# Kernel tuning notes

Measured on AMD Instinct MI355X. Metric: run time of the kernel, lower is better.

The kernel has to match this reference:

```python
import jax, jax.numpy as jnp
import numpy as np
from jax import lax

S, B, D_IN, H, T = 512, 256, 202, 100, 19  # seq, batch, input, hidden, tags


def setup_inputs() -> dict:
    key = jax.random.key(0)
    ks = jax.random.split(key, 16)
    sc = 0.1
    inp = {
        "x": jax.random.normal(ks[0], (S, B, D_IN), dtype=jnp.float32),
        "y": jax.random.randint(ks[1], (S, B), 0, T, dtype=jnp.int64),
        # forward-direction RNN params
        "W_ih_f": jax.random.normal(ks[2], (H, D_IN), dtype=jnp.float32) * sc,
        "W_hh_f": jax.random.normal(ks[3], (H, H), dtype=jnp.float32) * sc,
        "b_ih_f": jax.random.normal(ks[4], (H,), dtype=jnp.float32) * sc,
        "b_hh_f": jax.random.normal(ks[5], (H,), dtype=jnp.float32) * sc,
        # backward-direction RNN params
        "W_ih_b": jax.random.normal(ks[6], (H, D_IN), dtype=jnp.float32) * sc,
        "W_hh_b": jax.random.normal(ks[7], (H, H), dtype=jnp.float32) * sc,
        "b_ih_b": jax.random.normal(ks[8], (H,), dtype=jnp.float32) * sc,
        "b_hh_b": jax.random.normal(ks[9], (H,), dtype=jnp.float32) * sc,
        # tag projection
        "W_tag": jax.random.normal(ks[10], (T, 2 * H), dtype=jnp.float32) * sc,
        "b_tag": jax.random.normal(ks[11], (T,), dtype=jnp.float32) * sc,
        # CRF params
        "start_trans": jax.random.normal(ks[12], (T,), dtype=jnp.float32) * sc,
        "end_trans": jax.random.normal(ks[13], (T,), dtype=jnp.float32) * sc,
        "trans": jax.random.normal(ks[14], (T, T), dtype=jnp.float32) * sc,
    }
    return inp


def _rnn_dir(x, Wih, Whh, bih, bhh):
    # x: (S, B, D_IN) -> hs: (S, B, H), vanilla tanh RNN
    xp = jnp.einsum('sbd,hd->sbh', x, Wih) + bih + bhh
    h0 = jnp.zeros((x.shape[1], Wih.shape[0]), dtype=x.dtype)

    def step(h, xt):
        h = jnp.tanh(xt + h @ Whh.T)
        return h, h

    _, hs = lax.scan(step, h0, xp)
    return hs


def _crf_llh(emissions, tags, start_trans, end_trans, trans):
    # emissions: (N, L, T) batch_first; tags: (N, L). Returns sum log-likelihood.
    N, L, _ = emissions.shape
    # numerator: score of gold path
    em_score = jnp.take_along_axis(emissions, tags[..., None], axis=2)[..., 0].sum(axis=1)  # (N,)
    tr_score = trans[tags[:, :-1], tags[:, 1:]].sum(axis=1)  # (N,)
    numerator = start_trans[tags[:, 0]] + em_score + tr_score + end_trans[tags[:, -1]]
    # denominator: forward algorithm (log partition)
    alpha0 = start_trans + emissions[:, 0]  # (N, T)
    em_rest = jnp.swapaxes(emissions, 0, 1)[1:]  # (L-1, N, T)

    def step(alpha, em_t):
        # alpha: (N, T); broadcast over next-tag axis
        alpha = jax.nn.logsumexp(alpha[:, :, None] + trans[None] + em_t[:, None, :], axis=1)
        return alpha, None

    alpha, _ = lax.scan(step, alpha0, em_rest)
    denominator = jax.nn.logsumexp(alpha + end_trans, axis=1)  # (N,)
    return jnp.sum(numerator - denominator)


def reference(x, y, W_ih_f, W_hh_f, b_ih_f, b_hh_f, W_ih_b, W_hh_b, b_ih_b, b_hh_b,
              W_tag, b_tag, start_trans, end_trans, trans):
    # bidirectional RNN (seq-first, as nn.RNN default)
    h_fwd = _rnn_dir(x, W_ih_f, W_hh_f, b_ih_f, b_hh_f)
    h_bwd = _rnn_dir(x[::-1], W_ih_b, W_hh_b, b_ih_b, b_hh_b)[::-1]
    h = jnp.concatenate([h_fwd, h_bwd], axis=-1)  # (S, B, 200)
    logits = jnp.einsum('sbh,th->sbt', h, W_tag) + b_tag  # (S, B, 19)
    probs = jax.nn.softmax(logits, axis=2)
    # CRF was constructed with batch_first=True, so the (S,B,19) tensor is
    # treated as batch=S, seq=B (faithful to the original module's behavior).
    return _crf_llh(probs, y, start_trans, end_trans, trans)
```

## Files before the change

### kernel.cpp

```cpp
#include <hip/hip_runtime.h>
#include <math.h>

#define SS 512
#define BB 256
#define DIN 202
#define HH 100
#define TT 19

typedef short short8 __attribute__((ext_vector_type(8)));
typedef float f32x4 __attribute__((ext_vector_type(4)));

#define MFMA16(A, B, C) __builtin_amdgcn_mfma_f32_16x16x32_bf16(A, B, C, 0, 0, 0)

__device__ __forceinline__ float rl(float v, int i) {
    return __int_as_float(__builtin_amdgcn_readlane(__float_as_int(v), i));
}
__device__ __forceinline__ float rfl(float v) {
    return __int_as_float(__builtin_amdgcn_readfirstlane(__float_as_int(v)));
}
__device__ __forceinline__ unsigned short f2bf(float f) {
  unsigned u = __float_as_uint(f);
  u += 0x7fff + ((u >> 16) & 1);
  return (unsigned short)(u >> 16);
}
__device__ __forceinline__ float bf2f(unsigned v) {
  return __int_as_float((int)(v << 16));
}
__device__ __forceinline__ float fast_tanh(float z) {
  float e = __expf(2.f * z);
  return (e - 1.f) * __fdividef(1.f, e + 1.f);
}
__device__ __forceinline__ void gl_lds16(const void* g, void* l) {
  __builtin_amdgcn_global_load_lds(
      (const __attribute__((address_space(1))) unsigned int*)g,
      (__attribute__((address_space(3))) unsigned int*)l, 16, 0, 0);
}
__device__ __forceinline__ unsigned cvt_pk_bf16(float lo, float hi) {
  unsigned r;
  asm("v_cvt_pk_bf16_f32 %0, %1, %2" : "=v"(r) : "v"(lo), "v"(hi));
  return r;
}
__device__ __forceinline__ uint2 pack_tanh_pk(f32x4 a) {
  float h0 = fast_tanh(a[0]), h1 = fast_tanh(a[1]);
  float h2 = fast_tanh(a[2]), h3 = fast_tanh(a[3]);
  uint2 v;
  v.x = cvt_pk_bf16(h0, h1);
  v.y = cvt_pk_bf16(h2, h3);
  return v;
}
__device__ __forceinline__ uint2 pack_raw_pk(f32x4 a) {
  uint2 v;
  v.x = cvt_pk_bf16(a[0], a[1]);
  v.y = cvt_pk_bf16(a[2], a[3]);
  return v;
}
__device__ __forceinline__ f32x4 seed_from(const void* base, int off) {
  uint2 s = *(const uint2*)((const char*)base + off);
  return (f32x4){bf2f(s.x & 0xffffu), bf2f(s.x >> 16),
                 bf2f(s.y & 0xffffu), bf2f(s.y >> 16)};
}

__global__ __launch_bounds__(256) void k_cvtW(
    const float* __restrict__ Wf, const float* __restrict__ Wb,
    unsigned short* __restrict__ Wfrag) {
  int w = blockIdx.x * 256 + threadIdx.x;
  if (w >= 7 * 13 * 64) return;
  int kc = w / (13 * 64);
  int r = w % (13 * 64);
  int ft = r >> 6, l = r & 63;
  int nn = ft * 16 + (l & 15);
  int kb = kc * 32 + (l >> 4) * 8;
  union { unsigned short s[8]; int4 v; } pk;
  #pragma unroll
  for (int e = 0; e < 8; ++e) {
    int k = kb + e;
    float vv = 0.f;
    if (k < DIN) {
      if (nn < 100) vv = Wf[(size_t)nn * DIN + k];
      else if (nn < 200) vv = Wb[(size_t)(nn - 100) * DIN + k];
    }
    pk.s[e] = f2bf(vv);
  }
  *(int4*)&Wfrag[(size_t)w * 8] = pk.v;
}

__global__ __launch_bounds__(256) void k_inproj(
    const float* __restrict__ x, const unsigned short* __restrict__ Wfrag,
    const float* __restrict__ bihf, const float* __restrict__ bhhf,
    const float* __restrict__ bihb, const float* __restrict__ bhhb,
    unsigned short* __restrict__ xpT0, unsigned short* __restrict__ xpT1) {
  __shared__ __align__(16) char smem_raw[28672];
  __shared__ float lbias[208];
  short* lA = (short*)smem_raw;
  short* lB = (short*)(smem_raw + 8192);
  const int t = threadIdx.x;
  const int m0 = blockIdx.x * 128;
  const int s_idx = m0 >> 8;
  const int bhalf = (m0 >> 7) & 1;
  const int wv = t >> 6, lane = t & 63;
  const int li = lane & 15;

  if (t < 208) {
    float bv = 0.f;
    if (t < 100) bv = bihf[t] + bhhf[t];
    else if (t < 200) bv = bihb[t - 100] + bhhb[t - 100];
    lbias[t] = bv;
  }

  f32x4 acc[2][13];
  #pragma unroll
  for (int mf = 0; mf < 2; ++mf)
    #pragma unroll
    for (int nf = 0; nf < 13; ++nf)
      acc[mf][nf] = (f32x4){0.f, 0.f, 0.f, 0.f};

  for (int kc = 0; kc < 7; ++kc) {
    const int k0 = kc * 32;
    __syncthreads();
    #pragma unroll
    for (int j = 0; j < 8; ++j) {
      int g = t + 256 * j;
      int row = g >> 4, cp = g & 15;
      int col = k0 + cp * 2;
      unsigned pk2 = 0;
      if (col + 1 < DIN) {
        float2 v = *(const float2*)(x + (size_t)(m0 + row) * DIN + col);
        pk2 = cvt_pk_bf16(v.x, v.y);
      }
      int ft = row >> 4, i = row & 15;
      int kq = cp >> 2, e = (cp & 3) * 2;
      *(unsigned*)&lA[ft * 512 + (kq * 16 + i) * 8 + e] = pk2;
    }
    #pragma unroll
    for (int i = 0; i < 4; ++i) {
      int j = i * 4 + wv;
      if (j < 13)
        gl_lds16(Wfrag + ((size_t)(kc * 13 + j)) * 512, &lB[j * 512]);
    }
    __syncthreads();
    short8 a0 = *(const short8*)&lA[(2 * wv + 0) * 512 + lane * 8];
    short8 a1 = *(const short8*)&lA[(2 * wv + 1) * 512 + lane * 8];
    #pragma unroll
    for (int nf = 0; nf < 13; ++nf) {
      short8 b = *(const short8*)&lB[nf * 512 + lane * 8];
      acc[0][nf] = MFMA16(a0, b, acc[0][nf]);
      acc[1][nf] = MFMA16(a1, b, acc[1][nf]);
    }
  }
  __syncthreads();
  unsigned short* ep = (unsigned short*)smem_raw;
  float biasv[13];
  #pragma unroll
  for (int nf = 0; nf < 13; ++nf) biasv[nf] = lbias[nf * 16 + li];
  const int r0 = (lane >> 4) * 4;
  #pragma unroll
  for (int d = 0; d < 2; ++d) {
    if (d == 1) __syncthreads();
    #pragma unroll
    for (int mf = 0; mf < 2; ++mf) {
      int lrb = (2 * wv + mf) * 16 + r0;
      #pragma unroll
      for (int nf = 0; nf < 13; ++nf) {
        int col = nf * 16 + li;
        int c = col - 100 * d;
        if (c >= 0 && c < 100) {
          #pragma unroll
          for (int r = 0; r < 4; ++r)
            ep[(lrb + r) * 112 + c] = f2bf(acc[mf][nf][r] + biasv[nf]);
        }
      }
    }
    __syncthreads();
    unsigned short* dst0 = d ? xpT1 : xpT0;
    #pragma unroll
    for (int it = 0; it < 7; ++it) {
      int u = t + 256 * it;
      if (u < 1664) {
        int bgrpL = u / 208;
        int rem = u - bgrpL * 208;
        int u8 = rem >> 4, nn = rem & 15;
        int lr = bgrpL * 16 + nn;
        int4 v = *(const int4*)&ep[lr * 112 + u8 * 8];
        size_t off = ((((size_t)s_idx * 16 + bhalf * 8 + bgrpL) * 13 + u8) * 16 + nn) * 8;
        *(int4*)(dst0 + off) = v;
      }
    }
  }
}

__global__ __launch_bounds__(576) void k_rnn(
    const unsigned short* __restrict__ xpT0, const unsigned short* __restrict__ xpT1,
    const float* __restrict__ Whf, const float* __restrict__ Whb,
    const float* __restrict__ Wtag, float* __restrict__ plogF, float* __restrict__ plogB) {
  const int bid = blockIdx.x;
  const int dir = bid & 1;
  const int bgrp = (bid >> 1) & 15;
  const int b0 = bgrp * 16;
  const int seg = bid >> 5;
  const int start = (seg == 0) ? 0 : (64 * seg - 32);
  const int nch = (64 * seg + 64 - start) >> 3;
  const int outbase = 64 * seg;

  const float* Whh = dir ? Whb : Whf;
  const unsigned short* xpX = dir ? xpT1 : xpT0;
  float* plog = dir ? plogB : plogF;

  __shared__ short ringc[9][3][512];
  __shared__ short ring3[9][128];
  __shared__ unsigned short xpl[13312];
  __shared__ unsigned short larc[8 * 16 * 20];
  __shared__ short dummy16[8];

  const int t = threadIdx.x;
  const int wv = t >> 6, lane = t & 63;
  const int n = lane & 15, q = lane >> 4;

  for (int i = t; i < 3 * 512; i += 576) ringc[0][i >> 9][i & 511] = 0;
  for (int i = t; i < 9 * 128; i += 576) ring3[i >> 7][i & 127] = 0;
  if (t < 8) dummy16[t] = 0;

  short8 af[4];
  #pragma unroll
  for (int q2 = 0; q2 < 4; ++q2) af[q2] = (short8){0,0,0,0,0,0,0,0};
  {
    const float* base = nullptr;
    if (wv < 7) {
      int m = 16 * wv + n;
      if (m < HH) base = Whh + (size_t)m * HH;
    } else if (wv == 7) {
      if (n < TT) base = Wtag + (size_t)n * (2 * HH) + dir * HH;
    } else {
      int tA = 16 + n;
      if (tA < TT) base = Wtag + (size_t)tA * (2 * HH) + dir * HH;
    }
    #pragma unroll
    for (int q2 = 0; q2 < 4; ++q2) {
      union { unsigned short s[8]; short8 v; } pa;
      #pragma unroll
      for (int e = 0; e < 8; ++e) {
        int k = 32 * q2 + 8 * q + e;
        pa.s[e] = (base && k < HH) ? f2bf(base[k]) : 0;
      }
      af[q2] = pa.v;
    }
  }

  int slj[3], remj[3];
  #pragma unroll
  for (int i = 0; i < 3; ++i) {
    int j = i * 9 + wv;
    int jj = (j < 26) ? j : 0;
    int unit = jj * 64 + lane;
    slj[i] = unit / 208;
    remj[i] = unit - slj[i] * 208;
  }

  const int offW = ((2 * wv + (q >> 1)) * 16 + n) * 16 + (q & 1) * 8;

  for (int cc = 0; cc < nch; ++cc) {
    if (cc > 0) {
      if (t < 128) {
        int sl = t >> 4, nn2 = t & 15;
        int hs = start + (cc - 1) * 8 - 1 + sl;
        if (hs >= outbase) {
          int pos = dir ? (511 - hs) : hs;
          float* dst = plog + ((size_t)pos * 256 + b0 + nn2) * 20;
          const unsigned short* src = &larc[(sl * 16 + nn2) * 20];
          #pragma unroll
          for (int j5 = 0; j5 < 5; ++j5) {
            uint2 rv = *(const uint2*)&src[j5 * 4];
            float4 o;
            o.x = bf2f(rv.x & 0xffffu); o.y = bf2f(rv.x >> 16);
            o.z = bf2f(rv.y & 0xffffu); o.w = bf2f(rv.y >> 16);
            *(float4*)&dst[j5 * 4] = o;
          }
        }
      }
      if (t < 192) {
        *(int4*)&ringc[0][t >> 6][(t & 63) * 8] = *(const int4*)&ringc[8][t >> 6][(t & 63) * 8];
      } else if (t < 208) {
        int i2 = t - 192;
        *(int4*)&ring3[0][i2 * 8] = *(const int4*)&ring3[8][i2 * 8];
      }
    }
    #pragma unroll
    for (int i = 0; i < 3; ++i) {
      int j = i * 9 + wv;
      if (j < 26) {
        int s = start + cc * 8 + slj[i];
        int sq = dir ? (511 - s) : s;
        gl_lds16(xpX + (((size_t)sq * 16 + bgrp) * 208 + remj[i]) * 8, &xpl[j * 512]);
      }
    }
    __syncthreads();

    #pragma unroll
    for (int sl = 0; sl < 8; ++sl) {
      short8 hc0 = *(const short8*)&ringc[sl][0][lane * 8];
      short8 hc1 = *(const short8*)&ringc[sl][1][lane * 8];
      short8 hc2 = *(const short8*)&ringc[sl][2][lane * 8];
      short8 hc3 = *(const short8*)((q == 0) ? &ring3[sl][n * 8] : &dummy16[0]);
      f32x4 z4 = {0.f, 0.f, 0.f, 0.f};
      if (wv < 7) {
        int oW = sl * 3328 + offW;
        if (oW > 26616) oW = 26616;
        f32x4 seed = seed_from(xpl, oW);
        f32x4 a0 = MFMA16(af[0], hc0, seed);
        f32x4 a1 = MFMA16(af[1], hc1, z4);
        a0 = MFMA16(af[2], hc2, a0);
        a1 = MFMA16(af[3], hc3, a1);
        f32x4 a = a0 + a1;
        uint2 val = pack_tanh_pk(a);
        if (wv < 6) {
          *(uint2*)&ringc[sl + 1][wv >> 1][((2 * (wv & 1) + (q >> 1)) * 16 + n) * 8 + 4 * (q & 1)] = val;
        } else if (q == 0) {
          *(uint2*)&ring3[sl + 1][n * 8] = val;
        }
      } else {
        f32x4 a0 = MFMA16(af[0], hc0, z4);
        f32x4 a1 = MFMA16(af[1], hc1, z4);
        a0 = MFMA16(af[2], hc2, a0);
        a1 = MFMA16(af[3], hc3, a1);
        f32x4 a = a0 + a1;
        uint2 v = pack_raw_pk(a);
        if (wv == 7) {
          *(uint2*)&larc[(sl * 16 + n) * 20 + 4 * q] = v;
        } else if (q == 0) {
          *(uint2*)&larc[(sl * 16 + n) * 20 + 16] = v;
        }
      }
      __syncthreads();
    }
  }
  {
    if (t < 128) {
      int sl = t >> 4, nn2 = t & 15;
      int hs = start + (nch - 1) * 8 - 1 + sl;
      if (hs >= outbase) {
        int pos = dir ? (511 - hs) : hs;
        float* dst = plog + ((size_t)pos * 256 + b0 + nn2) * 20;
        const unsigned short* src = &larc[(sl * 16 + nn2) * 20];
        #pragma unroll
        for (int j5 = 0; j5 < 5; ++j5) {
          uint2 rv = *(const uint2*)&src[j5 * 4];
          float4 o;
          o.x = bf2f(rv.x & 0xffffu); o.y = bf2f(rv.x >> 16);
          o.z = bf2f(rv.y & 0xffffu); o.w = bf2f(rv.y >> 16);
          *(float4*)&dst[j5 * 4] = o;
        }
      }
    }
  }
  if (wv >= 7) {
    short8 hc0 = *(const short8*)&ringc[8][0][lane * 8];
    short8 hc1 = *(const short8*)&ringc[8][1][lane * 8];
    short8 hc2 = *(const short8*)&ringc[8][2][lane * 8];
    short8 hc3 = *(const short8*)((q == 0) ? &ring3[8][n * 8] : &dummy16[0]);
    f32x4 z4 = {0.f, 0.f, 0.f, 0.f};
    f32x4 a0 = MFMA16(af[0], hc0, z4);
    f32x4 a1 = MFMA16(af[1], hc1, z4);
    a0 = MFMA16(af[2], hc2, a0);
    a1 = MFMA16(af[3], hc3, a1);
    f32x4 a = a0 + a1;
    int hs = start + nch * 8 - 1;
    int pos = dir ? (511 - hs) : hs;
    float* dst = plog + ((size_t)pos * 256 + b0 + n) * 20;
    if (wv == 7) {
      #pragma unroll
      for (int r = 0; r < 4; ++r) dst[4 * q + r] = a[r];
    } else if (q == 0) {
      #pragma unroll
      for (int r = 0; r < 4; ++r) dst[16 + r] = a[r];
    }
  }
}

__global__ __launch_bounds__(256) void k_crf(
    const float* __restrict__ plogF, const float* __restrict__ plogB,
    const float* __restrict__ btag, const int* __restrict__ y,
    const float* __restrict__ start, const float* __restrict__ endt,
    const float* __restrict__ trans, float* __restrict__ out) {
  __shared__ float ltr[TT * TT];
  __shared__ float ltb[20];
  __shared__ float lem[4][64 * 21];
  const int t = threadIdx.x;
  const int wave = t >> 6, lane = t & 63;
  const int n = blockIdx.x * 4 + wave;
  for (int i = t; i < TT * TT; i += 256) ltr[i] = trans[i];
  if (t < 20) ltb[t] = (t < TT) ? btag[t] : 0.f;
  __syncthreads();
  const int* yn = y + n * BB;
  float Ereg[TT];
  #pragma unroll
  for (int i = 0; i < TT; ++i) Ereg[i] = (lane < TT) ? __expf(ltr[i * TT + lane]) : 0.f;
  float num = 0.f;
  float alpha = -1e30f;
  for (int c = 0; c < 4; ++c) {
    const size_t gbase = ((size_t)n * BB + c * 64) * 20;
    for (int u = lane; u < 1280; u += 64) {
      int row = u / 20, col = u - row * 20;
      lem[wave][row * 21 + col] = plogF[gbase + u] + plogB[gbase + u] + ltb[col];
    }
    {
      float vv[TT];
      float mx = -1e30f;
      #pragma unroll
      for (int j = 0; j < TT; ++j) { vv[j] = lem[wave][lane * 21 + j]; mx = fmaxf(mx, vv[j]); }
      float ssum = 0.f;
      #pragma unroll
      for (int j = 0; j < TT; ++j) { vv[j] = __expf(vv[j] - mx); ssum += vv[j]; }
      float inv = __fdividef(1.f, ssum);
      #pragma unroll
      for (int j = 0; j < TT; ++j) lem[wave][lane * 21 + j] = vv[j] * inv;
    }
    {
      int l = c * 64 + lane;
      int yt = yn[l];
      num += lem[wave][lane * 21 + yt];
      if (l < BB - 1) num += ltr[yt * TT + yn[l + 1]];
    }
    int llstart = 0;
    if (c == 0) {
      alpha = (lane < TT) ? (start[lane] + lem[wave][lane]) : -1e30f;
      llstart = 1;
    }
    for (int ll = llstart; ll < 64; ++ll) {
      float m = rfl(alpha);
      float ea = __expf(alpha - m);
      float s0 = 0.f, s1 = 0.f;
      #pragma unroll
      for (int i = 0; i < TT; i += 2) {
        s0 = fmaf(rl(ea, i), Ereg[i], s0);
        if (i + 1 < TT) s1 = fmaf(rl(ea, i + 1), Ereg[i + 1], s1);
      }
      float ssum = s0 + s1;
      float em_l = (lane < TT) ? lem[wave][ll * 21 + lane] : 0.f;
      alpha = em_l + m + __logf(ssum);
    }
  }
  #pragma unroll
  for (int o = 1; o < 64; o <<= 1) num += __shfl_xor(num, o);
  float av = alpha + ((lane < TT) ? endt[lane] : 0.f);
  float m2 = rfl(av);
  float ex = (lane < TT) ? __expf(av - m2) : 0.f;
  #pragma unroll
  for (int o = 1; o < 64; o <<= 1) ex += __shfl_xor(ex, o);
  if (lane == 0) {
    float denom = m2 + __logf(ex);
    float res = (start[yn[0]] + endt[yn[BB - 1]] + num) - denom;
    atomicAdd(out, res);
  }
}

extern "C" void kernel_launch(void* const* d_in, const int* in_sizes, int n_in,
                              void* d_out, int out_size, void* d_ws, size_t ws_size,
                              hipStream_t stream) {
  const float* x     = (const float*)d_in[0];
  const int*   y     = (const int*)d_in[1];
  const float* Wihf  = (const float*)d_in[2];
  const float* Whhf  = (const float*)d_in[3];
  const float* bihf  = (const float*)d_in[4];
  const float* bhhf  = (const float*)d_in[5];
  const float* Wihb  = (const float*)d_in[6];
  const float* Whhb  = (const float*)d_in[7];
  const float* bihb  = (const float*)d_in[8];
  const float* bhhb  = (const float*)d_in[9];
  const float* Wtag  = (const float*)d_in[10];
  const float* btag  = (const float*)d_in[11];
  const float* stt   = (const float*)d_in[12];
  const float* endt  = (const float*)d_in[13];
  const float* trans = (const float*)d_in[14];

  char* w = (char*)d_ws;
  unsigned short* Wfrag = (unsigned short*)w;  w += 128 * 1024;
  unsigned short* xpT0  = (unsigned short*)w;  w += (size_t)512 * 16 * 208 * 16;
  unsigned short* xpT1  = (unsigned short*)w;  w += (size_t)512 * 16 * 208 * 16;
  float* plogF = (float*)w;  w += (size_t)131072 * 20 * 4;
  float* plogB = (float*)w;  w += (size_t)131072 * 20 * 4;

  hipMemsetAsync(d_out, 0, sizeof(float) * out_size, stream);

  k_cvtW<<<23, 256, 0, stream>>>(Wihf, Wihb, Wfrag);
  k_inproj<<<1024, 256, 0, stream>>>(x, Wfrag, bihf, bhhf, bihb, bhhb, xpT0, xpT1);
  k_rnn<<<256, 576, 0, stream>>>(xpT0, xpT1, Whhf, Whhb, Wtag, plogF, plogB);
  k_crf<<<128, 256, 0, stream>>>(plogF, plogB, btag, y, stt, endt, trans, (float*)d_out);
}
```

Before: 365.7 us.

## Double-buffer input-projection GEMM tiles and prefetch next K-chunk during MFMA

The input-projection kernel now keeps two LDS buffers for the A (x) and B (weight) tiles. The next K-chunk's global loads are issued before the current chunk's MFMAs run, and the converted A tile is written after them, leaving one barrier per iteration instead of two. A loads are also widened to eight contiguous floats per thread. This should hide global-load latency behind compute, at the cost of more LDS (about 43KB) and registers, which may lower occupancy.

```diff
diff --git a/kernel.cpp b/kernel.cpp
--- a/kernel.cpp
+++ b/kernel.cpp
@@ -89,10 +89,8 @@
     const float* __restrict__ bihf, const float* __restrict__ bhhf,
     const float* __restrict__ bihb, const float* __restrict__ bhhb,
     unsigned short* __restrict__ xpT0, unsigned short* __restrict__ xpT1) {
-  __shared__ __align__(16) char smem_raw[28672];
+  __shared__ __align__(16) char smem_raw[43008];
   __shared__ float lbias[208];
-  short* lA = (short*)smem_raw;
-  short* lB = (short*)(smem_raw + 8192);
   const int t = threadIdx.x;
   const int m0 = blockIdx.x * 128;
   const int s_idx = m0 >> 8;
@@ -100,6 +98,9 @@
   const int wv = t >> 6, lane = t & 63;
   const int li = lane & 15;
 
+  short* lAb[2] = {(short*)smem_raw, (short*)(smem_raw + 21504)};
+  short* lBb[2] = {(short*)(smem_raw + 8192), (short*)(smem_raw + 29696)};
+
   if (t < 208) {
     float bv = 0.f;
     if (t < 100) bv = bihf[t] + bhhf[t];
@@ -114,40 +115,76 @@
     for (int nf = 0; nf < 13; ++nf)
       acc[mf][nf] = (f32x4){0.f, 0.f, 0.f, 0.f};
 
+  const int u0ft = t >> 6, u0ul = t & 63;
+  const int u1ft = (t + 256) >> 6, u1ul = (t + 256) & 63;
+  const int rowA[2] = {m0 + u0ft * 16 + (u0ul & 15), m0 + u1ft * 16 + (u1ul & 15)};
+  const int kqA[2] = {u0ul >> 4, u1ul >> 4};
+  const int dstA[2] = {u0ft * 512 + u0ul * 8, u1ft * 512 + u1ul * 8};
+
+  float2 va[2][4];
+
+  auto issueA = [&](int kc) {
+    #pragma unroll
+    for (int r = 0; r < 2; ++r) {
+      int kbase = kc * 32 + kqA[r] * 8;
+      const float* src = x + (size_t)rowA[r] * DIN + kbase;
+      if (kbase + 7 < DIN) {
+        va[r][0] = *(const float2*)(src);
+        va[r][1] = *(const float2*)(src + 2);
+        va[r][2] = *(const float2*)(src + 4);
+        va[r][3] = *(const float2*)(src + 6);
+      } else {
+        #pragma unroll
+        for (int e2 = 0; e2 < 4; ++e2) {
+          float x0 = (kbase + 2 * e2 < DIN) ? src[2 * e2] : 0.f;
+          float x1 = (kbase + 2 * e2 + 1 < DIN) ? src[2 * e2 + 1] : 0.f;
+          va[r][e2] = make_float2(x0, x1);
+        }
+      }
+    }
+  };
+  auto writeA = [&](int buf) {
+    #pragma unroll
+    for (int r = 0; r < 2; ++r) {
+      union { unsigned w[4]; int4 v; } pk;
+      #pragma unroll
+      for (int e2 = 0; e2 < 4; ++e2)
+        pk.w[e2] = cvt_pk_bf16(va[r][e2].x, va[r][e2].y);
+      *(int4*)&lAb[buf][dstA[r]] = pk.v;
+    }
+  };
+  auto issueB = [&](int kc, int buf) {
+    #pragma unroll
+    for (int i2 = 0; i2 < 4; ++i2) {
+      int j = i2 * 4 + wv;
+      if (j < 13)
+        gl_lds16(Wfrag + ((size_t)(kc * 13 + j)) * 512, &lBb[buf][j * 512]);
+    }
+  };
+
+  issueA(0);
+  issueB(0, 0);
+  writeA(0);
+  __syncthreads();
+
   for (int kc = 0; kc < 7; ++kc) {
-    const int k0 = kc * 32;
-    __syncthreads();
-    #pragma unroll
-    for (int j = 0; j < 8; ++j) {
-      int g = t + 256 * j;
-      int row = g >> 4, cp = g & 15;
-      int col = k0 + cp * 2;
-      unsigned pk2 = 0;
-      if (col + 1 < DIN) {
-        float2 v = *(const float2*)(x + (size_t)(m0 + row) * DIN + col);
-        pk2 = cvt_pk_bf16(v.x, v.y);
-      }
-      int ft = row >> 4, i = row & 15;
-      int kq = cp >> 2, e = (cp & 3) * 2;
-      *(unsigned*)&lA[ft * 512 + (kq * 16 + i) * 8 + e] = pk2;
-    }
-    #pragma unroll
-    for (int i = 0; i < 4; ++i) {
-      int j = i * 4 + wv;
-      if (j < 13)
-        gl_lds16(Wfrag + ((size_t)(kc * 13 + j)) * 512, &lB[j * 512]);
-    }
-    __syncthreads();
-    short8 a0 = *(const short8*)&lA[(2 * wv + 0) * 512 + lane * 8];
-    short8 a1 = *(const short8*)&lA[(2 * wv + 1) * 512 + lane * 8];
+    const int cur = kc & 1, nxt = cur ^ 1;
+    if (kc < 6) {
+      issueA(kc + 1);
+      issueB(kc + 1, nxt);
+    }
+    short8 a0 = *(const short8*)&lAb[cur][(2 * wv + 0) * 512 + lane * 8];
+    short8 a1 = *(const short8*)&lAb[cur][(2 * wv + 1) * 512 + lane * 8];
     #pragma unroll
     for (int nf = 0; nf < 13; ++nf) {
-      short8 b = *(const short8*)&lB[nf * 512 + lane * 8];
+      short8 b = *(const short8*)&lBb[cur][nf * 512 + lane * 8];
       acc[0][nf] = MFMA16(a0, b, acc[0][nf]);
       acc[1][nf] = MFMA16(a1, b, acc[1][nf]);
     }
-  }
-  __syncthreads();
+    if (kc < 6) writeA(nxt);
+    __syncthreads();
+  }
+
   unsigned short* ep = (unsigned short*)smem_raw;
   float biasv[13];
   #pragma unroll
```

Result: faster. 339.2 us (-7.2%).
